# Performance work log

Hardware: AMD Instinct MI355X
Metric: run time of the kernel (lower is better)

Reference implementation:

```python
import jax, jax.numpy as jnp
import numpy as np

NUM_FRAMES = 64
H, W = 2048, 2048
MAX_DEPTH = 12


def setup_inputs() -> dict:
    key = jax.random.key(0)
    k1, k2, k3 = jax.random.split(key, 3)
    frame_colors = jax.random.uniform(k1, (NUM_FRAMES, 3), dtype=jnp.float32)
    frame_selection = jax.random.uniform(k2, (NUM_FRAMES, 2, NUM_FRAMES), dtype=jnp.float32)
    split_ratios = jax.random.uniform(k3, (NUM_FRAMES,), dtype=jnp.float32)
    return {
        "frame_colors": frame_colors,
        "frame_selection": frame_selection,
        "split_ratios": split_ratios,
    }


def reference(frame_colors, frame_selection, split_ratios):
    """Vectorized per-pixel descent of the bounded fractal recursion.

    Instead of recursive slice-assignments with host-synced argmax/.item(),
    each pixel tracks (frame idx, region origin, region size) and descends
    MAX_DEPTH levels via gathers. Equivalent math to render_frame(0,...).
    """
    # Per-frame child indices (argmax over the selection logits).
    left_child = jnp.argmax(frame_selection[:, 0, :], axis=-1).astype(jnp.int32)   # [F]
    right_child = jnp.argmax(frame_selection[:, 1, :], axis=-1).astype(jnp.int32)  # [F]

    yy, xx = jnp.meshgrid(jnp.arange(H, dtype=jnp.int32),
                          jnp.arange(W, dtype=jnp.int32), indexing="ij")  # [H,W]

    idx = jnp.zeros((H, W), jnp.int32)   # current frame index per pixel
    y0 = jnp.zeros((H, W), jnp.int32)    # region origin
    x0 = jnp.zeros((H, W), jnp.int32)
    h = jnp.full((H, W), H, jnp.int32)   # region size
    w = jnp.full((H, W), W, jnp.int32)
    done = jnp.zeros((H, W), bool)

    for _ in range(MAX_DEPTH):
        leaf = (w < 2) | (h < 2)            # base case: region too small
        act = (~done) & (~leaf)             # pixels that descend this level
        done = done | leaf

        ratio = split_ratios[idx]                       # [H,W]
        is_vert = (idx % 2) == 1                        # split_directions = i % 2
        # left_width = max(1, int(width * ratio)); analogous top_height
        lw = jnp.maximum(1, jnp.floor(w.astype(jnp.float32) * ratio).astype(jnp.int32))
        th = jnp.maximum(1, jnp.floor(h.astype(jnp.float32) * ratio).astype(jnp.int32))

        go_left = jnp.where(is_vert, (xx - x0) < lw, (yy - y0) < th)
        child = jnp.where(go_left, left_child[idx], right_child[idx])

        nx0 = jnp.where(is_vert & (~go_left), x0 + lw, x0)
        nw = jnp.where(is_vert, jnp.where(go_left, lw, w - lw), w)
        ny0 = jnp.where((~is_vert) & (~go_left), y0 + th, y0)
        nh = jnp.where(~is_vert, jnp.where(go_left, th, h - th), h)

        idx = jnp.where(act, child, idx)
        x0 = jnp.where(act, nx0, x0)
        w = jnp.where(act, nw, w)
        y0 = jnp.where(act, ny0, y0)
        h = jnp.where(act, nh, h)

    # Fill each pixel with its leaf frame's background color -> [3, H, W]
    out = frame_colors[idx]                 # [H, W, 3]
    return jnp.transpose(out, (2, 0, 1))
```

## Files before the change

kernel.cpp:

```cpp
#include <hip/hip_runtime.h>

#define HH_DIM 2048
#define WW_DIM 2048
#define NF 64
#define MAX_DEPTH 12
#define NBLK 16
#define SEG 8192

__device__ __forceinline__ uint2 enc(int x0, int y0, int idx, int w, int h) {
    return make_uint2((unsigned)x0 | ((unsigned)y0 << 12) | ((unsigned)idx << 24),
                      (unsigned)w | ((unsigned)h << 12));
}

__device__ __forceinline__ unsigned wave_iscan(unsigned x, int lane) {
    #pragma unroll
    for (int off = 1; off < 64; off <<= 1) {
        unsigned v = __shfl_up(x, off);
        if (lane >= off) x += v;
    }
    return x;
}

__global__ __launch_bounds__(256)
void build_kernel(const float* __restrict__ sel,
                  const float* __restrict__ ratios,
                  const float* __restrict__ colors,
                  float4* __restrict__ cpack,
                  int* __restrict__ cnt,
                  uint2* __restrict__ items) {
    __shared__ float s_ratio[NF];
    __shared__ int   s_child[2 * NF];
    __shared__ int   s_items;

    int t = threadIdx.x;
    int lane = t & 63;

    if (t < 2 * NF) {
        const float* row = sel + t * NF;
        float best = row[0]; int bi = 0;
        #pragma unroll
        for (int j = 1; j < NF; ++j) { float v = row[j]; if (v > best) { best = v; bi = j; } }
        s_child[t] = bi;
    }
    if (t < NF) {
        s_ratio[t] = ratios[t];
        if (blockIdx.x == 0)
            cpack[t] = make_float4(colors[3*t], colors[3*t+1], colors[3*t+2], 0.0f);
    }
    if (t == 0) s_items = 0;
    __syncthreads();

    int j = (blockIdx.x << 8) + t;
    int x0 = 0, y0 = 0, w = WW_DIM, h = HH_DIM, idx = 0;
    bool alive = true;
    #pragma unroll
    for (int d = 0; d < MAX_DEPTH; ++d) {
        int bit = (j >> (11 - d)) & 1;
        if (w < 2 || h < 2) {
            if (bit) { alive = false; break; }
            continue;
        }
        float ratio = s_ratio[idx];
        if (idx & 1) {
            int lw = (int)floorf((float)w * ratio); if (lw < 1) lw = 1;
            if (bit == 0) { w = lw; } else { x0 += lw; w -= lw; }
        } else {
            int th = (int)floorf((float)h * ratio); if (th < 1) th = 1;
            if (bit == 0) { h = th; } else { y0 += th; h -= th; }
        }
        idx = bit ? s_child[2 * idx + 1] : s_child[2 * idx];
    }

    unsigned nit = 0;
    int rpc = 1;
    if (alive) {
        rpc = 1024 / w; if (rpc < 1) rpc = 1;
        nit = (unsigned)((h + rpc - 1) / rpc);
    }

    unsigned inc = wave_iscan(nit, lane);
    unsigned tot = __shfl(inc, 63);
    int base = 0;
    if (lane == 63 && tot) base = atomicAdd(&s_items, (int)tot);
    base = __shfl(base, 63);
    int s = base + (int)(inc - nit);

    uint2* seg = items + blockIdx.x * SEG;
    if (nit) {
        int nn = (int)nit;
        for (int k = 0; k < nn; ++k) {
            int r0 = k * rpc;
            int hc = h - r0; if (hc > rpc) hc = rpc;
            if (s + k < SEG) seg[s + k] = enc(x0, y0 + r0, idx, w, hc);
        }
    }
    __syncthreads();
    if (t == 0) cnt[blockIdx.x] = (s_items < SEG) ? s_items : SEG;
}

__global__ __launch_bounds__(256)
void fill_kernel(const float4* __restrict__ cpack,
                 const int* __restrict__ cnt,
                 const uint2* __restrict__ items,
                 float* __restrict__ out) {
    const int plane = HH_DIM * WW_DIM;
    for (int slot = blockIdx.x; slot < NBLK * SEG; slot += gridDim.x) {
        int sg = slot / SEG, li = slot - sg * SEG;
        if (li >= cnt[sg]) continue;
        uint2 v = items[slot];
        int x0 = (int)(v.x & 0xFFF), y0 = (int)((v.x >> 12) & 0xFFF);
        int idx = (int)(v.x >> 24);
        int w = (int)(v.y & 0xFFF), hc = (int)((v.y >> 12) & 0xFFF);
        float4 col = cpack[idx];
        int n = w * hc;
        float rw = 1.0f / (float)w;
        for (int p = threadIdx.x; p < n; p += 256) {
            int r = (int)((float)p * rw);
            int c = p - r * w;
            if (c < 0)       { r -= 1; c += w; }
            else if (c >= w) { r += 1; c -= w; }
            int off = (y0 + r) * WW_DIM + x0 + c;
            out[off]             = col.x;
            out[plane + off]     = col.y;
            out[2 * plane + off] = col.z;
        }
    }
}

extern "C" void kernel_launch(void* const* d_in, const int* in_sizes, int n_in,
                              void* d_out, int out_size, void* d_ws, size_t ws_size,
                              hipStream_t stream) {
    const float* frame_colors    = (const float*)d_in[0];
    const float* frame_selection = (const float*)d_in[1];
    const float* split_ratios    = (const float*)d_in[2];
    float* out = (float*)d_out;

    float4* cpack = (float4*)d_ws;
    int*    cnt   = (int*)((char*)d_ws + 1024);
    uint2*  items = (uint2*)((char*)d_ws + 1088);

    build_kernel<<<NBLK, 256, 0, stream>>>(frame_selection, split_ratios,
                                           frame_colors, cpack, cnt, items);
    fill_kernel<<<4096, 256, 0, stream>>>(cpack, cnt, items, out);
}
```

Baseline: 110.0 us.

## Split fill into byte index-map paint and vectorized colorize pass

The region fill now writes a one-byte frame index per pixel into a workspace map instead of three scattered float stores. A new colorize kernel reads four indices at a time and writes coalesced float4 stores to all three planes from shared-memory color tables. The paint kernel walks a compacted item list using per-segment prefix offsets instead of scanning all slots, and items are chunked at 2048 pixels instead of 1024. This adds a third launch and an extra map write and read pass in exchange for fully coalesced output writes.

```diff
diff --git a/kernel.cpp b/kernel.cpp
--- a/kernel.cpp
+++ b/kernel.cpp
@@ -6,6 +6,7 @@
 #define MAX_DEPTH 12
 #define NBLK 16
 #define SEG 8192
+#define CHUNK 2048
 
 __device__ __forceinline__ uint2 enc(int x0, int y0, int idx, int w, int h) {
     return make_uint2((unsigned)x0 | ((unsigned)y0 << 12) | ((unsigned)idx << 24),
@@ -24,8 +25,6 @@
 __global__ __launch_bounds__(256)
 void build_kernel(const float* __restrict__ sel,
                   const float* __restrict__ ratios,
-                  const float* __restrict__ colors,
-                  float4* __restrict__ cpack,
                   int* __restrict__ cnt,
                   uint2* __restrict__ items) {
     __shared__ float s_ratio[NF];
@@ -42,11 +41,7 @@
         for (int j = 1; j < NF; ++j) { float v = row[j]; if (v > best) { best = v; bi = j; } }
         s_child[t] = bi;
     }
-    if (t < NF) {
-        s_ratio[t] = ratios[t];
-        if (blockIdx.x == 0)
-            cpack[t] = make_float4(colors[3*t], colors[3*t+1], colors[3*t+2], 0.0f);
-    }
+    if (t < NF) s_ratio[t] = ratios[t];
     if (t == 0) s_items = 0;
     __syncthreads();
 
@@ -74,7 +69,7 @@
     unsigned nit = 0;
     int rpc = 1;
     if (alive) {
-        rpc = 1024 / w; if (rpc < 1) rpc = 1;
+        rpc = CHUNK / w; if (rpc < 1) rpc = 1;
         nit = (unsigned)((h + rpc - 1) / rpc);
     }
 
@@ -99,32 +94,57 @@
 }
 
 __global__ __launch_bounds__(256)
-void fill_kernel(const float4* __restrict__ cpack,
-                 const int* __restrict__ cnt,
-                 const uint2* __restrict__ items,
-                 float* __restrict__ out) {
-    const int plane = HH_DIM * WW_DIM;
-    for (int slot = blockIdx.x; slot < NBLK * SEG; slot += gridDim.x) {
-        int sg = slot / SEG, li = slot - sg * SEG;
-        if (li >= cnt[sg]) continue;
-        uint2 v = items[slot];
+void paint_kernel(const int* __restrict__ cnt,
+                  const uint2* __restrict__ items,
+                  unsigned char* __restrict__ map) {
+    int pre[NBLK];
+    int total = 0;
+    #pragma unroll
+    for (int s = 0; s < NBLK; ++s) { pre[s] = total; total += cnt[s]; }
+
+    for (int r = blockIdx.x; r < total; r += gridDim.x) {
+        int sg = 0;
+        #pragma unroll
+        for (int s = 1; s < NBLK; ++s) if (r >= pre[s]) sg = s;
+        uint2 v = items[sg * SEG + (r - pre[sg])];
         int x0 = (int)(v.x & 0xFFF), y0 = (int)((v.x >> 12) & 0xFFF);
-        int idx = (int)(v.x >> 24);
+        unsigned char idx = (unsigned char)(v.x >> 24);
         int w = (int)(v.y & 0xFFF), hc = (int)((v.y >> 12) & 0xFFF);
-        float4 col = cpack[idx];
         int n = w * hc;
         float rw = 1.0f / (float)w;
         for (int p = threadIdx.x; p < n; p += 256) {
-            int r = (int)((float)p * rw);
-            int c = p - r * w;
-            if (c < 0)       { r -= 1; c += w; }
-            else if (c >= w) { r += 1; c -= w; }
-            int off = (y0 + r) * WW_DIM + x0 + c;
-            out[off]             = col.x;
-            out[plane + off]     = col.y;
-            out[2 * plane + off] = col.z;
+            int rr = (int)((float)p * rw);
+            int c = p - rr * w;
+            if (c < 0)       { rr -= 1; c += w; }
+            else if (c >= w) { rr += 1; c -= w; }
+            map[(y0 + rr) * WW_DIM + x0 + c] = idx;
         }
     }
+}
+
+__global__ __launch_bounds__(256)
+void colorize_kernel(const float* __restrict__ colors,
+                     const unsigned char* __restrict__ map,
+                     float* __restrict__ out) {
+    __shared__ float s_r[NF], s_g[NF], s_b[NF];
+    int t = threadIdx.x;
+    if (t < NF) {
+        s_r[t] = colors[3 * t];
+        s_g[t] = colors[3 * t + 1];
+        s_b[t] = colors[3 * t + 2];
+    }
+    __syncthreads();
+
+    int gid = blockIdx.x * 256 + t;
+    unsigned m4 = *(const unsigned*)(map + gid * 4);
+    int i0 = (int)(m4 & 0xFF), i1 = (int)((m4 >> 8) & 0xFF);
+    int i2 = (int)((m4 >> 16) & 0xFF), i3 = (int)(m4 >> 24);
+
+    int base = gid * 4;
+    const int plane = HH_DIM * WW_DIM;
+    *(float4*)(out + base)             = make_float4(s_r[i0], s_r[i1], s_r[i2], s_r[i3]);
+    *(float4*)(out + plane + base)     = make_float4(s_g[i0], s_g[i1], s_g[i2], s_g[i3]);
+    *(float4*)(out + 2 * plane + base) = make_float4(s_b[i0], s_b[i1], s_b[i2], s_b[i3]);
 }
 
 extern "C" void kernel_launch(void* const* d_in, const int* in_sizes, int n_in,
@@ -135,11 +155,12 @@
     const float* split_ratios    = (const float*)d_in[2];
     float* out = (float*)d_out;
 
-    float4* cpack = (float4*)d_ws;
-    int*    cnt   = (int*)((char*)d_ws + 1024);
-    uint2*  items = (uint2*)((char*)d_ws + 1088);
+    int*           cnt   = (int*)d_ws;
+    uint2*         items = (uint2*)((char*)d_ws + 1024);
+    unsigned char* map   = (unsigned char*)((char*)d_ws + (2 << 20));
 
     build_kernel<<<NBLK, 256, 0, stream>>>(frame_selection, split_ratios,
-                                           frame_colors, cpack, cnt, items);
-    fill_kernel<<<4096, 256, 0, stream>>>(cpack, cnt, items, out);
+                                           cnt, items);
+    paint_kernel<<<4096, 256, 0, stream>>>(cnt, items, map);
+    colorize_kernel<<<4096, 256, 0, stream>>>(frame_colors, map, out);
 }
```

Result: faster. 100.1 us (-9.0%).
